# Optimization experiments

Measured on AMD Instinct MI355X. Metric: run time of the kernel, lower is better.

## Reference

```python
import jax, jax.numpy as jnp
import numpy as np

D, H, E, TAU = 1024, 2048, 8, 0.1
X_SHAPE = (2, 2048, D)
N = X_SHAPE[0] * X_SHAPE[1]


def setup_inputs() -> dict:
    key = jax.random.key(0)
    ks = jax.random.split(key, 12)
    s_in = 1.0 / np.sqrt(D)
    s_hid = 1.0 / np.sqrt(H)
    return {
        "x": jax.random.normal(ks[0], X_SHAPE, jnp.float32),
        "gumbel_u": jax.random.uniform(ks[1], (N, E), jnp.float32, 1e-6, 1.0 - 1e-6),
        "eps": jax.random.normal(ks[2], (N, E, D), jnp.float32),
        "Wg1": jax.random.normal(ks[3], (D, H), jnp.float32) * s_in,
        "bg1": jnp.zeros((H,), jnp.float32),
        "Wg2": jax.random.normal(ks[4], (H, E), jnp.float32) * s_hid,
        "bg2": jnp.zeros((E,), jnp.float32),
        "Wm1": jax.random.normal(ks[5], (E, D, H), jnp.float32) * s_in,
        "bm1": jnp.zeros((E, H), jnp.float32),
        "Wm2": jax.random.normal(ks[6], (E, H, D), jnp.float32) * s_hid,
        "bm2": jnp.zeros((E, D), jnp.float32),
        "Wv1": jax.random.normal(ks[7], (E, D, H), jnp.float32) * s_in,
        "bv1": jnp.zeros((E, H), jnp.float32),
        "Wv2": jax.random.normal(ks[8], (E, H, D), jnp.float32) * s_hid,
        "bv2": jnp.zeros((E, D), jnp.float32),
    }


def reference(x, gumbel_u, eps, Wg1, bg1, Wg2, bg2, Wm1, bm1, Wm2, bm2, Wv1, bv1, Wv2, bv2):
    orig_shape = x.shape
    xf = x.reshape(-1, D)  # [N, D]

    # Gate: Linear -> ReLU -> Linear, then soft Gumbel-Softmax
    gate_logits = jax.nn.relu(xf @ Wg1 + bg1) @ Wg2 + bg2  # [N, E]
    gumbel = -jnp.log(-jnp.log(gumbel_u))
    w = jax.nn.softmax((gate_logits + gumbel) / TAU, axis=-1)  # [N, E]

    # Per-expert 2-layer MLPs, batched over the expert axis as grouped GEMMs
    hm = jax.nn.relu(jnp.einsum("nd,edh->neh", xf, Wm1) + bm1)
    mus = jnp.einsum("neh,ehd->ned", hm, Wm2) + bm2  # [N, E, D]
    hv = jax.nn.relu(jnp.einsum("nd,edh->neh", xf, Wv1) + bv1)
    logvars = jnp.einsum("neh,ehd->ned", hv, Wv2) + bv2  # [N, E, D]

    # Reparameterized sample per expert, then gate-weighted sum over experts
    samples = mus + eps * jnp.exp(0.5 * logvars)  # [N, E, D]
    out = jnp.einsum("ne,ned->nd", w, samples)  # [N, D]
    return out.reshape(orig_shape)
```

## Files before the change

### kernel.cpp

```cpp
#include <hip/hip_runtime.h>


typedef _Float16 f16x8 __attribute__((ext_vector_type(8)));
typedef float    f32x4 __attribute__((ext_vector_type(4)));

__device__ __forceinline__ void async_copy16(const void* g, void* l) {
  __builtin_amdgcn_global_load_lds(
      (const __attribute__((address_space(1))) void*)g,
      (__attribute__((address_space(3))) void*)l, 16, 0, 0);
}

#define MFMA16(a_, b_, c_) __builtin_amdgcn_mfma_f32_16x16x32_f16(a_, b_, c_, 0, 0, 0)


__global__ __launch_bounds__(256) void split_x_kernel(
    const float* __restrict__ x, _Float16* __restrict__ Ax) {
  int idx = blockIdx.x * 256 + threadIdx.x;
  int m = idx >> 10, k = idx & 1023;
  float v = x[idx];
  _Float16 hi = (_Float16)v;
  _Float16 lo = (_Float16)(v - (float)hi);
  _Float16* row = Ax + (size_t)m * 3072;
  row[k] = hi;
  row[k + 1024] = hi;
  row[k + 2048] = lo;
}

__global__ __launch_bounds__(256) void split_transpose_wg1_kernel(
    const float* __restrict__ in, _Float16* __restrict__ out) {
  __shared__ float tile[64][65];
  int kb = blockIdx.y * 64, nb = blockIdx.x * 64;
  int c = threadIdx.x & 63, r0 = threadIdx.x >> 6;
#pragma unroll
  for (int i = 0; i < 16; ++i) {
    int r = r0 + i * 4;
    tile[r][c] = in[(size_t)(kb + r) * 2048 + nb + c];
  }
  __syncthreads();
#pragma unroll
  for (int i = 0; i < 16; ++i) {
    int rn = r0 + i * 4;
    float v = tile[c][rn];
    _Float16 hi = (_Float16)v;
    _Float16 lo = (_Float16)(v - (float)hi);
    _Float16* row = out + (size_t)(nb + rn) * 3072 + kb;
    row[c] = hi;
    row[c + 1024] = lo;
    row[c + 2048] = hi;
  }
}

__global__ __launch_bounds__(256) void transpose_f32_to_f16(
    const float* __restrict__ in, _Float16* __restrict__ out, int K, int N) {
  __shared__ float tile[64][65];
  size_t zo = (size_t)blockIdx.z * K * N;
  int kb = blockIdx.y * 64, nb = blockIdx.x * 64;
  int c = threadIdx.x & 63, r0 = threadIdx.x >> 6;
  const float* ip = in + zo + (size_t)kb * N + nb;
#pragma unroll
  for (int i = 0; i < 16; ++i) {
    int r = r0 + i * 4;
    tile[r][c] = ip[(size_t)r * N + c];
  }
  __syncthreads();
  _Float16* op = out + zo + (size_t)nb * K + kb;
#pragma unroll
  for (int i = 0; i < 16; ++i) {
    int rn = r0 + i * 4;
    op[(size_t)rn * K + c] = (_Float16)tile[c][rn];
  }
}

__global__ __launch_bounds__(256) void zero_out_kernel(float4* __restrict__ p) {
  p[blockIdx.x * 256 + threadIdx.x] = float4{0.f, 0.f, 0.f, 0.f};
}

__device__ __forceinline__ void gemm256_acc(
    const _Float16* __restrict__ Abase, const int lda,
    const _Float16* __restrict__ Bbase, const int ldb,
    const int NT, _Float16* lds, f32x4 (&acc)[8][4]) {
  const int tid = threadIdx.x;
  const int lane = tid & 63, wid = tid >> 6;
  const int wm = wid >> 2, wn = wid & 3;
  const int lanelo = lane & 15, laneq = lane >> 4;
  const int colp0 = (laneq * 8) ^ ((lanelo & 7) << 3);
  const int rowoffA = (wm * 128 + lanelo) * 64;
  const int rowoffB = (wn * 64 + lanelo) * 64;

  _Float16* const As0 = lds;
  _Float16* const As1 = lds + 16384;
  _Float16* const Bs0 = lds + 32768;
  _Float16* const Bs1 = lds + 49152;

  const int sr = tid >> 3;
  const int sc = ((tid & 7) ^ (sr & 7)) << 3;
  const size_t goffA = (size_t)sr * lda + sc;
  const size_t goffB = (size_t)sr * ldb + sc;
  const size_t rowsA64 = (size_t)64 * lda;
  const size_t rowsB64 = (size_t)64 * ldb;
  const int tid8 = tid * 8;

#define STAGE_A(dstbuf, kp, hf)                                  \
  do {                                                           \
    const _Float16* g_ = (kp) + (size_t)(hf)*2 * rowsA64 + goffA;\
    _Float16* d_ = (dstbuf) + (hf)*8192 + tid8;                  \
    async_copy16(g_, d_);                                        \
    async_copy16(g_ + rowsA64, d_ + 4096);                       \
  } while (0)
#define STAGE_B(dstbuf, kp, hf)                                  \
  do {                                                           \
    const _Float16* g_ = (kp) + (size_t)(hf)*2 * rowsB64 + goffB;\
    _Float16* d_ = (dstbuf) + (hf)*8192 + tid8;                  \
    async_copy16(g_, d_);                                        \
    async_copy16(g_ + rowsB64, d_ + 4096);                       \
  } while (0)
#define BARRIER() asm volatile("s_barrier" ::: "memory")

  const _Float16* aN = Abase + 64;
  const _Float16* bN = Bbase + 128;

  STAGE_A(As0, Abase, 0);
  STAGE_A(As0, Abase, 1);
  STAGE_B(Bs0, Bbase, 0);
  STAGE_B(Bs0, Bbase, 1);
  STAGE_B(Bs1, Bbase + 64, 0);
  STAGE_B(Bs1, Bbase + 64, 1);
  asm volatile("s_waitcnt vmcnt(4)" ::: "memory");
  BARRIER();

  for (int kt = 0; kt < NT; ++kt) {
    _Float16* const bufA = (kt & 1) ? As1 : As0;
    _Float16* const bufB = (kt & 1) ? Bs1 : Bs0;
    _Float16* const nxtA = (kt & 1) ? As0 : As1;
    const _Float16* const rA0 = bufA + rowoffA + colp0;
    const _Float16* const rA1 = bufA + rowoffA + (colp0 ^ 32);
    const _Float16* const rB0 = bufB + rowoffB + colp0;
    const _Float16* const rB1 = bufB + rowoffB + (colp0 ^ 32);
    const bool st1 = (kt + 1 < NT), st2 = (kt + 2 < NT);
    f16x8 a[4][2], b[4][2];

#pragma unroll
    for (int i = 0; i < 4; ++i) {
      a[i][0] = *(const f16x8*)(rA0 + i * 1024);
      a[i][1] = *(const f16x8*)(rA1 + i * 1024);
    }
#pragma unroll
    for (int j = 0; j < 2; ++j) {
      b[j][0] = *(const f16x8*)(rB0 + j * 1024);
      b[j][1] = *(const f16x8*)(rB1 + j * 1024);
    }
    if (st1) STAGE_A(nxtA, aN, 0);
    BARRIER();
    __builtin_amdgcn_sched_barrier(0);
    __builtin_amdgcn_s_setprio(1);
#pragma unroll
    for (int i = 0; i < 4; ++i)
#pragma unroll
      for (int j = 0; j < 2; ++j) {
        acc[i][j] = MFMA16(a[i][0], b[j][0], acc[i][j]);
        acc[i][j] = MFMA16(a[i][1], b[j][1], acc[i][j]);
      }
    __builtin_amdgcn_s_setprio(0);
    __builtin_amdgcn_sched_barrier(0);
    BARRIER();

#pragma unroll
    for (int j = 0; j < 2; ++j) {
      b[2 + j][0] = *(const f16x8*)(rB0 + (2 + j) * 1024);
      b[2 + j][1] = *(const f16x8*)(rB1 + (2 + j) * 1024);
    }
    if (st1) STAGE_A(nxtA, aN, 1);
    BARRIER();
    __builtin_amdgcn_sched_barrier(0);
    __builtin_amdgcn_s_setprio(1);
#pragma unroll
    for (int i = 0; i < 4; ++i)
#pragma unroll
      for (int j = 0; j < 2; ++j) {
        acc[i][2 + j] = MFMA16(a[i][0], b[2 + j][0], acc[i][2 + j]);
        acc[i][2 + j] = MFMA16(a[i][1], b[2 + j][1], acc[i][2 + j]);
      }
    __builtin_amdgcn_s_setprio(0);
    __builtin_amdgcn_sched_barrier(0);
    BARRIER();

#pragma unroll
    for (int i = 0; i < 4; ++i) {
      a[i][0] = *(const f16x8*)(rA0 + 4096 + i * 1024);
      a[i][1] = *(const f16x8*)(rA1 + 4096 + i * 1024);
    }
    if (st2) STAGE_B(bufB, bN, 0);
    BARRIER();
    __builtin_amdgcn_sched_barrier(0);
    __builtin_amdgcn_s_setprio(1);
#pragma unroll
    for (int i = 0; i < 4; ++i)
#pragma unroll
      for (int j = 0; j < 2; ++j) {
        acc[4 + i][j] = MFMA16(a[i][0], b[j][0], acc[4 + i][j]);
        acc[4 + i][j] = MFMA16(a[i][1], b[j][1], acc[4 + i][j]);
      }
    __builtin_amdgcn_s_setprio(0);
    __builtin_amdgcn_sched_barrier(0);
    BARRIER();

    if (st2) STAGE_B(bufB, bN, 1);
    BARRIER();
    __builtin_amdgcn_sched_barrier(0);
    __builtin_amdgcn_s_setprio(1);
#pragma unroll
    for (int i = 0; i < 4; ++i)
#pragma unroll
      for (int j = 0; j < 2; ++j) {
        acc[4 + i][2 + j] = MFMA16(a[i][0], b[2 + j][0], acc[4 + i][2 + j]);
        acc[4 + i][2 + j] = MFMA16(a[i][1], b[2 + j][1], acc[4 + i][2 + j]);
      }
    __builtin_amdgcn_s_setprio(0);
    __builtin_amdgcn_sched_barrier(0);
    if (st2) {
      asm volatile("s_waitcnt vmcnt(4)" ::: "memory");
    } else {
      asm volatile("s_waitcnt vmcnt(0)" ::: "memory");
    }
    BARRIER();

    aN += 64;
    bN += 64;
  }
#undef STAGE_A
#undef STAGE_B
#undef BARRIER
}

__global__ __launch_bounds__(512, 2) void gate_gemm1_256(
    const _Float16* __restrict__ A, const _Float16* __restrict__ Bt,
    float* __restrict__ C, const float* __restrict__ bias) {
  extern __shared__ _Float16 lds[];
  const int m0 = blockIdx.y * 256, n0 = blockIdx.x * 256;
  f32x4 acc[8][4] = {};
  gemm256_acc(A + (size_t)m0 * 3072, 3072, Bt + (size_t)n0 * 3072, 3072, 48,
              lds, acc);
  const int tid = threadIdx.x, lane = tid & 63, wid = tid >> 6;
  const int wm = wid >> 2, wn = wid & 3;
  const int lanelo = lane & 15, laneq = lane >> 4;
#pragma unroll
  for (int nf = 0; nf < 4; ++nf) {
    const int n = n0 + wn * 64 + nf * 16 + lanelo;
    const float bn = bias[n];
#pragma unroll
    for (int mf = 0; mf < 8; ++mf)
#pragma unroll
      for (int r = 0; r < 4; ++r) {
        const int m = m0 + wm * 128 + mf * 16 + laneq * 4 + r;
        float v = acc[mf][nf][r] + bn;
        C[(size_t)m * 2048 + n] = v > 0.f ? v : 0.f;
      }
  }
}

__global__ __launch_bounds__(512, 2) void expert_gemm1_256(
    const _Float16* __restrict__ A, const _Float16* __restrict__ W1t,
    _Float16* __restrict__ hm, _Float16* __restrict__ hv,
    const float* __restrict__ bm1, const float* __restrict__ bv1) {
  extern __shared__ _Float16 lds[];
  const int z = blockIdx.z, e = z & 7, s = z >> 3;
  const _Float16* __restrict__ Bt = W1t + (size_t)z * 2048 * 1024;
  _Float16* __restrict__ C = (s ? hv : hm) + (size_t)e * 4096 * 2048;
  const float* __restrict__ bias = (s ? bv1 : bm1) + e * 2048;
  const int m0 = blockIdx.y * 256, n0 = blockIdx.x * 256;
  f32x4 acc[8][4] = {};
  gemm256_acc(A + (size_t)m0 * 3072, 3072, Bt + (size_t)n0 * 1024, 1024, 16,
              lds, acc);
  const int tid = threadIdx.x, lane = tid & 63, wid = tid >> 6;
  const int wm = wid >> 2, wn = wid & 3;
  const int lanelo = lane & 15, laneq = lane >> 4;
#pragma unroll
  for (int nf = 0; nf < 4; ++nf) {
    const int n = n0 + wn * 64 + nf * 16 + lanelo;
    const float bn = bias[n];
#pragma unroll
    for (int mf = 0; mf < 8; ++mf)
#pragma unroll
      for (int r = 0; r < 4; ++r) {
        const int m = m0 + wm * 128 + mf * 16 + laneq * 4 + r;
        float v = acc[mf][nf][r] + bn;
        C[(size_t)m * 2048 + n] = (_Float16)(v > 0.f ? v : 0.f);
      }
  }
}

__global__ __launch_bounds__(512, 2) void gemm2_combine_256(
    const _Float16* __restrict__ hm, const _Float16* __restrict__ hv,
    const _Float16* __restrict__ W2t, const float* __restrict__ bm2,
    const float* __restrict__ bv2, const float* __restrict__ eps,
    const float* __restrict__ w, float* __restrict__ out) {
  extern __shared__ _Float16 lds[];
  const int e = blockIdx.z;
  const _Float16* __restrict__ Am = hm + (size_t)e * 4096 * 2048;
  const _Float16* __restrict__ Av = hv + (size_t)e * 4096 * 2048;
  const _Float16* __restrict__ Btm = W2t + (size_t)e * 1024 * 2048;
  const _Float16* __restrict__ Btv = W2t + (size_t)(8 + e) * 1024 * 2048;
  const float* __restrict__ bmb = bm2 + e * 1024;
  const float* __restrict__ bvb = bv2 + e * 1024;
  const int m0 = blockIdx.y * 256, n0 = blockIdx.x * 256;
  const int tid = threadIdx.x, lane = tid & 63, wid = tid >> 6;
  const int wm = wid >> 2, wn = wid & 3;
  const int lanelo = lane & 15, laneq = lane >> 4;

  f32x4 acc[8][4] = {};
  gemm256_acc(Av + (size_t)m0 * 2048, 2048, Btv + (size_t)n0 * 2048, 2048, 32,
              lds, acc);
#pragma unroll
  for (int nf = 0; nf < 4; ++nf) {
    const int d = n0 + wn * 64 + nf * 16 + lanelo;
    const float bvd = bvb[d];
    const float bmd = bmb[d];
#pragma unroll
    for (int mf = 0; mf < 8; ++mf)
#pragma unroll
      for (int r = 0; r < 4; ++r) {
        const int m = m0 + wm * 128 + mf * 16 + laneq * 4 + r;
        const float ev = eps[(size_t)m * 8192 + e * 1024 + d];
        acc[mf][nf][r] = ev * __expf(0.5f * (acc[mf][nf][r] + bvd)) + bmd;
      }
  }
  asm volatile("s_barrier" ::: "memory");
  gemm256_acc(Am + (size_t)m0 * 2048, 2048, Btm + (size_t)n0 * 2048, 2048, 32,
              lds, acc);
#pragma unroll
  for (int mf = 0; mf < 8; ++mf)
#pragma unroll
    for (int r = 0; r < 4; ++r) {
      const int m = m0 + wm * 128 + mf * 16 + laneq * 4 + r;
      const float wgt = w[(size_t)m * 8 + e];
      float* orow = out + (size_t)m * 1024;
#pragma unroll
      for (int nf = 0; nf < 4; ++nf) {
        const int d = n0 + wn * 64 + nf * 16 + lanelo;
        unsafeAtomicAdd(&orow[d], wgt * acc[mf][nf][r]);
      }
    }
}

__global__ __launch_bounds__(256) void gate_finish_kernel(
    const float* __restrict__ hg, const float* __restrict__ Wg2,
    const float* __restrict__ bg2, const float* __restrict__ gu,
    float* __restrict__ w) {
  const int lane = threadIdx.x & 63, wid = threadIdx.x >> 6;
  const int row = blockIdx.x * 4 + wid;
  const float* hrow = hg + (size_t)row * 2048;
  float acc[8] = {0.f, 0.f, 0.f, 0.f, 0.f, 0.f, 0.f, 0.f};
  for (int h = lane; h < 2048; h += 64) {
    const float hv = hrow[h];
    const float* wr = Wg2 + (size_t)h * 8;
#pragma unroll
    for (int e = 0; e < 8; ++e) acc[e] += hv * wr[e];
  }
#pragma unroll
  for (int off = 32; off > 0; off >>= 1) {
#pragma unroll
    for (int e = 0; e < 8; ++e) acc[e] += __shfl_down(acc[e], off);
  }
  if (lane == 0) {
    float z[8], zmax = -1e30f;
#pragma unroll
    for (int e = 0; e < 8; ++e) {
      const float u = gu[(size_t)row * 8 + e];
      const float g = -logf(-logf(u));
      z[e] = (acc[e] + bg2[e] + g) / 0.1f;
      zmax = fmaxf(zmax, z[e]);
    }
    float s = 0.f;
#pragma unroll
    for (int e = 0; e < 8; ++e) {
      z[e] = __expf(z[e] - zmax);
      s += z[e];
    }
    const float inv = 1.f / s;
#pragma unroll
    for (int e = 0; e < 8; ++e) w[(size_t)row * 8 + e] = z[e] * inv;
  }
}


extern "C" void kernel_launch(void* const* d_in, const int* in_sizes, int n_in,
                              void* d_out, int out_size, void* d_ws,
                              size_t ws_size, hipStream_t stream) {
  const float* x = (const float*)d_in[0];
  const float* gu = (const float*)d_in[1];
  const float* eps = (const float*)d_in[2];
  const float* Wg1 = (const float*)d_in[3];
  const float* bg1 = (const float*)d_in[4];
  const float* Wg2 = (const float*)d_in[5];
  const float* bg2 = (const float*)d_in[6];
  const float* Wm1 = (const float*)d_in[7];
  const float* bm1 = (const float*)d_in[8];
  const float* Wm2 = (const float*)d_in[9];
  const float* bm2 = (const float*)d_in[10];
  const float* Wv1 = (const float*)d_in[11];
  const float* bv1 = (const float*)d_in[12];
  const float* Wv2 = (const float*)d_in[13];
  const float* bv2 = (const float*)d_in[14];
  float* out = (float*)d_out;

  static bool attr_done = false;
  if (!attr_done) {
    (void)hipFuncSetAttribute((const void*)gate_gemm1_256,
                              hipFuncAttributeMaxDynamicSharedMemorySize,
                              131072);
    (void)hipFuncSetAttribute((const void*)expert_gemm1_256,
                              hipFuncAttributeMaxDynamicSharedMemorySize,
                              131072);
    (void)hipFuncSetAttribute((const void*)gemm2_combine_256,
                              hipFuncAttributeMaxDynamicSharedMemorySize,
                              131072);
    attr_done = true;
  }

  char* ws = (char*)d_ws;
  size_t off = 0;
  auto alloc = [&](size_t bytes) -> void* {
    void* p = ws + off;
    off = (off + bytes + 255) & ~(size_t)255;
    return p;
  };
  _Float16* Ax = (_Float16*)alloc(4096UL * 3072 * 2);
  _Float16* Wg1t = (_Float16*)alloc(2048UL * 3072 * 2);
  _Float16* W1t = (_Float16*)alloc(16UL * 2048 * 1024 * 2);
  _Float16* W2t = (_Float16*)alloc(16UL * 1024 * 2048 * 2);
  float* hg = (float*)alloc(4096UL * 2048 * 4);
  float* wbuf = (float*)alloc(4096UL * 8 * 4);
  _Float16* hm = (_Float16*)alloc(8UL * 4096 * 2048 * 2);
  _Float16* hv = (_Float16*)alloc(8UL * 4096 * 2048 * 2);

  zero_out_kernel<<<4096, 256, 0, stream>>>((float4*)out);
  split_x_kernel<<<4096 * 1024 / 256, 256, 0, stream>>>(x, Ax);
  split_transpose_wg1_kernel<<<dim3(2048 / 64, 1024 / 64), 256, 0, stream>>>(Wg1, Wg1t);
  transpose_f32_to_f16<<<dim3(2048 / 64, 1024 / 64, 8), 256, 0, stream>>>(
      Wm1, W1t, 1024, 2048);
  transpose_f32_to_f16<<<dim3(2048 / 64, 1024 / 64, 8), 256, 0, stream>>>(
      Wv1, W1t + 8UL * 2048 * 1024, 1024, 2048);
  transpose_f32_to_f16<<<dim3(1024 / 64, 2048 / 64, 8), 256, 0, stream>>>(
      Wm2, W2t, 2048, 1024);
  transpose_f32_to_f16<<<dim3(1024 / 64, 2048 / 64, 8), 256, 0, stream>>>(
      Wv2, W2t + 8UL * 1024 * 2048, 2048, 1024);

  gate_gemm1_256<<<dim3(2048 / 256, 4096 / 256), 512, 131072, stream>>>(
      Ax, Wg1t, hg, bg1);
  gate_finish_kernel<<<4096 / 4, 256, 0, stream>>>(hg, Wg2, bg2, gu, wbuf);

  expert_gemm1_256<<<dim3(2048 / 256, 4096 / 256, 16), 512, 131072, stream>>>(
      Ax, W1t, hm, hv, bm1, bv1);
  gemm2_combine_256<<<dim3(1024 / 256, 4096 / 256, 8), 512, 131072, stream>>>(
      hm, hv, W2t, bm2, bv2, eps, wbuf, out);
}
```

Before: 1.170 ms.

## Merge B staging phases, drop barrier, and add XCD-aware block swizzle

The GEMM main loop now issues both halves of the B staging together and runs the second A-half MFMAs over all four B column groups in one phase. This removes two barriers per K-iteration. Separately, all three GEMM kernels remap their flattened block id with an XCD swizzle, so blocks that share operand tiles land on the same XCD and can reuse its L2. Removing barriers risks LDS read/write hazards if the staging now overlaps reads still in flight.

```diff
diff --git a/kernel.cpp b/kernel.cpp
--- a/kernel.cpp
+++ b/kernel.cpp
@@ -11,6 +11,10 @@
 }
 
 #define MFMA16(a_, b_, c_) __builtin_amdgcn_mfma_f32_16x16x32_f16(a_, b_, c_, 0, 0, 0)
+
+__device__ __forceinline__ int xcd_swizzle(int id, int nwg) {
+  return (id & 7) * (nwg >> 3) + (id >> 3);
+}
 
 
 __global__ __launch_bounds__(256) void split_x_kernel(
@@ -162,7 +166,6 @@
       }
     __builtin_amdgcn_s_setprio(0);
     __builtin_amdgcn_sched_barrier(0);
-    BARRIER();
 
 #pragma unroll
     for (int j = 0; j < 2; ++j) {
@@ -189,31 +192,19 @@
       a[i][0] = *(const f16x8*)(rA0 + 4096 + i * 1024);
       a[i][1] = *(const f16x8*)(rA1 + 4096 + i * 1024);
     }
-    if (st2) STAGE_B(bufB, bN, 0);
+    if (st2) {
+      STAGE_B(bufB, bN, 0);
+      STAGE_B(bufB, bN, 1);
+    }
     BARRIER();
     __builtin_amdgcn_sched_barrier(0);
     __builtin_amdgcn_s_setprio(1);
 #pragma unroll
     for (int i = 0; i < 4; ++i)
 #pragma unroll
-      for (int j = 0; j < 2; ++j) {
+      for (int j = 0; j < 4; ++j) {
         acc[4 + i][j] = MFMA16(a[i][0], b[j][0], acc[4 + i][j]);
         acc[4 + i][j] = MFMA16(a[i][1], b[j][1], acc[4 + i][j]);
-      }
-    __builtin_amdgcn_s_setprio(0);
-    __builtin_amdgcn_sched_barrier(0);
-    BARRIER();
-
-    if (st2) STAGE_B(bufB, bN, 1);
-    BARRIER();
-    __builtin_amdgcn_sched_barrier(0);
-    __builtin_amdgcn_s_setprio(1);
-#pragma unroll
-    for (int i = 0; i < 4; ++i)
-#pragma unroll
-      for (int j = 0; j < 2; ++j) {
-        acc[4 + i][2 + j] = MFMA16(a[i][0], b[2 + j][0], acc[4 + i][2 + j]);
-        acc[4 + i][2 + j] = MFMA16(a[i][1], b[2 + j][1], acc[4 + i][2 + j]);
       }
     __builtin_amdgcn_s_setprio(0);
     __builtin_amdgcn_sched_barrier(0);
@@ -236,7 +227,9 @@
     const _Float16* __restrict__ A, const _Float16* __restrict__ Bt,
     float* __restrict__ C, const float* __restrict__ bias) {
   extern __shared__ _Float16 lds[];
-  const int m0 = blockIdx.y * 256, n0 = blockIdx.x * 256;
+  const int nid = xcd_swizzle(blockIdx.x + 8 * blockIdx.y, 128);
+  const int bx = nid & 7, by = nid >> 3;
+  const int m0 = by * 256, n0 = bx * 256;
   f32x4 acc[8][4] = {};
   gemm256_acc(A + (size_t)m0 * 3072, 3072, Bt + (size_t)n0 * 3072, 3072, 48,
               lds, acc);
@@ -263,11 +256,14 @@
     _Float16* __restrict__ hm, _Float16* __restrict__ hv,
     const float* __restrict__ bm1, const float* __restrict__ bv1) {
   extern __shared__ _Float16 lds[];
-  const int z = blockIdx.z, e = z & 7, s = z >> 3;
+  const int nid = xcd_swizzle(
+      blockIdx.x + 8 * (blockIdx.y + 16 * blockIdx.z), 2048);
+  const int bx = nid & 7, by = (nid >> 3) & 15, z = nid >> 7;
+  const int e = z & 7, s = z >> 3;
   const _Float16* __restrict__ Bt = W1t + (size_t)z * 2048 * 1024;
   _Float16* __restrict__ C = (s ? hv : hm) + (size_t)e * 4096 * 2048;
   const float* __restrict__ bias = (s ? bv1 : bm1) + e * 2048;
-  const int m0 = blockIdx.y * 256, n0 = blockIdx.x * 256;
+  const int m0 = by * 256, n0 = bx * 256;
   f32x4 acc[8][4] = {};
   gemm256_acc(A + (size_t)m0 * 3072, 3072, Bt + (size_t)n0 * 1024, 1024, 16,
               lds, acc);
@@ -295,14 +291,16 @@
     const float* __restrict__ bv2, const float* __restrict__ eps,
     const float* __restrict__ w, float* __restrict__ out) {
   extern __shared__ _Float16 lds[];
-  const int e = blockIdx.z;
+  const int nid = xcd_swizzle(
+      blockIdx.x + 4 * (blockIdx.y + 16 * blockIdx.z), 512);
+  const int bx = nid & 3, by = (nid >> 2) & 15, e = nid >> 6;
   const _Float16* __restrict__ Am = hm + (size_t)e * 4096 * 2048;
   const _Float16* __restrict__ Av = hv + (size_t)e * 4096 * 2048;
   const _Float16* __restrict__ Btm = W2t + (size_t)e * 1024 * 2048;
   const _Float16* __restrict__ Btv = W2t + (size_t)(8 + e) * 1024 * 2048;
   const float* __restrict__ bmb = bm2 + e * 1024;
   const float* __restrict__ bvb = bv2 + e * 1024;
-  const int m0 = blockIdx.y * 256, n0 = blockIdx.x * 256;
+  const int m0 = by * 256, n0 = bx * 256;
   const int tid = threadIdx.x, lane = tid & 63, wid = tid >> 6;
   const int wm = wid >> 2, wn = wid & 3;
   const int lanelo = lane & 15, laneq = lane >> 4;
```

After: 1.180 ms. Within noise of the previous version (+0.8%).
